# Kernel optimization log

Hardware: AMD Instinct MI355X
Metric: run time of the kernel (lower is better)

Reference implementation:

```python
import jax, jax.numpy as jnp
import numpy as np

SOS, EOS, PAD = 1, 2, 0


def setup_inputs() -> dict:
    key = jax.random.key(0)
    ks = jax.random.split(key, 8)
    n, d_z, d_h, d_emb, V = 8192, 128, 512, 128, 64
    s = lambda k, shape, scale: jax.random.normal(k, shape, jnp.float32) * scale
    return {
        "Z": jax.random.normal(ks[0], (n, d_z), jnp.float32),
        "emb": s(ks[1], (V, d_emb), 0.1),
        "z2h_w": s(ks[2], (d_h, d_z), 0.05),
        "z2h_b": jnp.zeros((d_h,), jnp.float32),
        "w_ih0": s(ks[3], (3 * d_h, d_emb), 0.05),
        "w_ih_rest": s(ks[4], (2, 3 * d_h, d_h), 0.05),
        "w_hh": s(ks[5], (3, 3 * d_h, d_h), 0.05),
        "b_ih": jnp.zeros((3, 3 * d_h), jnp.float32),
        "b_hh": jnp.zeros((3, 3 * d_h), jnp.float32),
        "h2v_w": s(ks[6], (V, d_h), 0.05),
        "h2v_b": jnp.zeros((V,), jnp.float32),
        "max_len": 80,
    }


def _gru_cell(x, h, w_ih, w_hh, b_ih, b_hh):
    # torch GRU gate order: r, z, n
    gi = x @ w_ih.T + b_ih
    gh = h @ w_hh.T + b_hh
    i_r, i_z, i_n = jnp.split(gi, 3, axis=-1)
    h_r, h_z, h_n = jnp.split(gh, 3, axis=-1)
    r = jax.nn.sigmoid(i_r + h_r)
    z = jax.nn.sigmoid(i_z + h_z)
    g = jnp.tanh(i_n + r * h_n)
    return (1.0 - z) * g + z * h


def _decode(Z, emb, z2h_w, z2h_b, w_ih0, w_ih_rest, w_hh, b_ih, b_hh, h2v_w, h2v_b, max_len):
    n = Z.shape[0]
    L = w_hh.shape[0]
    h0 = Z @ z2h_w.T + z2h_b                      # [n, d_h], repeated over layers
    H = jnp.broadcast_to(h0[None], (L,) + h0.shape)
    x0 = jnp.full((n,), SOS, jnp.int32)
    eos0 = jnp.zeros((n,), bool)
    w_ih = [w_ih0] + [w_ih_rest[i] for i in range(w_ih_rest.shape[0])]

    def step(carry, t):
        H, x_prev, eos = carry
        inp = emb[x_prev]                          # [n, d_emb]
        Hs = []
        for l in range(L):                         # small fixed layer loop
            h_new = _gru_cell(inp, H[l], w_ih[l], w_hh[l], b_ih[l], b_hh[l])
            Hs.append(h_new)
            inp = h_new
        probs = jax.nn.softmax(inp @ h2v_w.T + h2v_b, axis=-1)  # [n, V]
        x_t = jnp.argmax(probs, axis=-1).astype(jnp.int32)      # ModeSampler
        tok = jnp.where(eos, PAD, x_t)             # masked write into X_gen
        new_eos = (~eos) & (x_t == EOS)
        return (jnp.stack(Hs), x_t, eos | new_eos), (tok, new_eos, probs)

    ts = jnp.arange(1, max_len, dtype=jnp.int32)
    _, (toks, new_eos, probs) = jax.lax.scan(step, (H, x0, eos0), ts)
    X_gen = jnp.concatenate([jnp.full((n, 1), SOS, jnp.int32), toks.T], axis=1)  # [n, max_len]
    any_eos = new_eos.any(axis=0)
    first_t = ts[jnp.argmax(new_eos, axis=0)]
    seq_lens = jnp.where(any_eos, first_t + 1, max_len).astype(jnp.int32)
    return X_gen, seq_lens, probs


def reference(Z, emb, z2h_w, z2h_b, w_ih0, w_ih_rest, w_hh, b_ih, b_hh, h2v_w, h2v_b, max_len):
    X_gen, seq_lens, _ = _decode(Z, emb, z2h_w, z2h_b, w_ih0, w_ih_rest,
                                 w_hh, b_ih, b_hh, h2v_w, h2v_b, max_len)
    # torch returns a ragged list X_gen[i, :seq_lens[i]]; we return the padded
    # tensor plus lengths (jit-compatible equivalent).
    return X_gen, seq_lens
```

## Files before the change

### kernel.cpp

```cpp
#include <hip/hip_runtime.h>
#include <math.h>

#define NSEQ 8192
#define DH 512
#define DZ 128
#define DE 128
#define VOCAB 64
#define TMAX 80
#define SOS 1
#define EOS_TOK 2

#define TMR 64
#define TNCOL 32

typedef _Float16 half_t;
typedef half_t h8 __attribute__((ext_vector_type(8)));
typedef float f4 __attribute__((ext_vector_type(4)));

__device__ __forceinline__ float sigf(float x) { return 1.0f / (1.0f + expf(-x)); }

__device__ __forceinline__ void split2(float v, half_t& hi, half_t& lo) {
    float hf = (float)(half_t)v;
    if (fabsf(v) < 6.2e-5f) hf = 0.0f;
    hi = (half_t)hf;
    lo = (half_t)((v - hf) * 2048.0f);
}

__device__ __forceinline__ float rec2(half_t h, half_t l) {
    return (float)h + (float)l * (1.0f / 2048.0f);
}

__device__ __forceinline__ void gl_lds16(const void* g, void* l) {
    __builtin_amdgcn_global_load_lds((const __attribute__((address_space(1))) void*)g,
                                     (__attribute__((address_space(3))) void*)l, 16, 0, 0);
}

__device__ __forceinline__ void swizzle_rc(int bid, int& r, int& c) {
    const int x = bid & 7;
    const int q = bid >> 3;
    r = (q & 15) * 8 + x;
    c = q >> 4;
}

__global__ __launch_bounds__(256) void init_kernel(int* __restrict__ x_prev,
                                                   int* __restrict__ eos,
                                                   int* __restrict__ out,
                                                   int* __restrict__ list,
                                                   int* __restrict__ count) {
    int i = blockIdx.x * 256 + threadIdx.x;
    x_prev[i] = SOS;
    eos[i] = 0;
    list[i] = i;
    out[i * TMAX] = SOS;
    out[NSEQ * TMAX + i] = TMAX;
    if (i == 0) count[0] = NSEQ;
}

__global__ __launch_bounds__(1024) void compact_kernel(const int* __restrict__ eos,
                                                       int* __restrict__ list,
                                                       int* __restrict__ count) {
    __shared__ int part[1024];
    __shared__ int slist[NSEQ];
    const int tid = threadIdx.x;
    const int base = tid * 8;
    int f[8], s = 0;
#pragma unroll
    for (int i = 0; i < 8; ++i) { f[i] = eos[base + i] ? 0 : 1; s += f[i]; }
    part[tid] = s;
    __syncthreads();
    for (int off = 1; off < 1024; off <<= 1) {
        int v = (tid >= off) ? part[tid - off] : 0;
        __syncthreads();
        part[tid] += v;
        __syncthreads();
    }
    const int total = part[1023];
    int p = part[tid] - s;
#pragma unroll
    for (int i = 0; i < 8; ++i) if (f[i]) slist[p++] = base + i;
    __syncthreads();
    if (tid == 0) {
        count[0] = total;
        if (total > 0) {
            const int last = slist[total - 1];
            const int padn = (total + 63) & ~63;
            for (int k = total; k < padn; ++k) slist[k] = last;
        }
    }
    __syncthreads();
    const int padn = (total + 63) & ~63;
    for (int k = tid; k < padn; k += 1024) list[k] = slist[k];
}

__global__ __launch_bounds__(256) void h0_kernel(const float* __restrict__ Z,
                                                 const float* __restrict__ w,
                                                 const float* __restrict__ b,
                                                 half_t* __restrict__ B0h, half_t* __restrict__ B0l,
                                                 half_t* __restrict__ B1h, half_t* __restrict__ B1l,
                                                 half_t* __restrict__ B2h, half_t* __restrict__ B2l) {
    __shared__ float zrow[DZ];
    const int i = blockIdx.x;
    const int tid = threadIdx.x;
    if (tid < DZ) zrow[tid] = Z[(size_t)i * DZ + tid];
    __syncthreads();
    for (int j = tid; j < DH; j += 256) {
        double s = (double)b[j];
        const float* wr = w + (size_t)j * DZ;
#pragma unroll 8
        for (int k = 0; k < DZ; ++k) s += (double)zrow[k] * (double)wr[k];
        float sf = (float)s;
        half_t hi, lo;
        split2(sf, hi, lo);
        size_t o = (size_t)i * DH + j;
        B0h[o] = hi; B0l[o] = lo;
        B1h[o] = hi; B1l[o] = lo;
        B2h[o] = hi; B2l[o] = lo;
    }
}

__global__ __launch_bounds__(256) void gi0_kernel(const float* __restrict__ emb,
                                                  const float* __restrict__ w_ih0,
                                                  const float* __restrict__ b_ih0,
                                                  double* __restrict__ tab) {
    __shared__ float e[DE];
    const int x = blockIdx.x;
    const int tid = threadIdx.x;
    if (tid < DE) e[tid] = emb[(size_t)x * DE + tid];
    __syncthreads();
    for (int j = tid; j < 3 * DH; j += 256) {
        double s = (double)b_ih0[j];
        const float* wr = w_ih0 + (size_t)j * DE;
#pragma unroll 8
        for (int k = 0; k < DE; ++k) s += (double)e[k] * (double)wr[k];
        tab[(size_t)x * 3 * DH + j] = s;
    }
}

__global__ __launch_bounds__(256) void wsplit_kernel(const float* __restrict__ w,
                                                     half_t* __restrict__ hi,
                                                     half_t* __restrict__ lo, int n) {
    int i = blockIdx.x * 256 + threadIdx.x;
    if (i < n) {
        half_t h, l;
        split2(w[i], h, l);
        hi[i] = h; lo[i] = l;
    }
}


__global__ __launch_bounds__(256, 3) void layer0_mfma(
    const half_t* __restrict__ Hch, const half_t* __restrict__ Hcl,
    half_t* __restrict__ Hnh, half_t* __restrict__ Hnl,
    const half_t* __restrict__ Wh, const half_t* __restrict__ Wl,
    const float* __restrict__ b_hh0,
    const double* __restrict__ tab,
    const int* __restrict__ x_prev,
    const int* __restrict__ list, const int* __restrict__ count) {
    int rt, ct;
    swizzle_rc(blockIdx.x, rt, ct);
    const int row0 = rt * TMR;
    const int cnt = count[0];
    if (row0 >= cnt) return;
    const int col0 = ct * TNCOL;

    __shared__ char sm[40960];
    const int tid = threadIdx.x;
    const int lane = tid & 63, w = tid >> 6;
    const int lr = lane & 15, lq = lane >> 4;
    const int wr0 = (w >> 1) * 32, wc0 = (w & 1) * 16;

    int aoff[2], boff[3];
#pragma unroll
    for (int i = 0; i < 2; ++i) {
        int u = i * 256 + tid, r = u >> 3, s = u & 7;
        aoff[i] = list[row0 + r] * 1024 + ((s ^ (r & 7)) << 4);
    }
#pragma unroll
    for (int j = 0; j < 3; ++j) {
        int u = j * 256 + tid, br = u >> 3, s = u & 7;
        int wr = (br >> 5) * DH + col0 + (br & 31);
        boff[j] = wr * 1024 + ((s ^ (br & 7)) << 4);
    }

    int fa[2][2], fb[3][2];
#pragma unroll
    for (int rf = 0; rf < 2; ++rf)
#pragma unroll
        for (int ks = 0; ks < 2; ++ks) {
            int row = wr0 + rf * 16 + lr;
            int sb = ks * 4 + lq;
            fa[rf][ks] = row * 128 + ((sb ^ (row & 7)) << 4);
        }
#pragma unroll
    for (int g = 0; g < 3; ++g)
#pragma unroll
        for (int ks = 0; ks < 2; ++ks) {
            int br = g * 32 + wc0 + lr;
            int sb = ks * 4 + lq;
            fb[g][ks] = br * 128 + ((sb ^ (br & 7)) << 4);
        }

    f4 hh[2][3] = {}, cc[2][3] = {};
    const char* Ah = (const char*)Hch;
    const char* Al = (const char*)Hcl;
    const char* Bh = (const char*)Wh;
    const char* Bl = (const char*)Wl;

    for (int kc = 0; kc < 8; ++kc) {
        const int kb = kc * 128;
#pragma unroll
        for (int i = 0; i < 2; ++i) {
            gl_lds16(Ah + aoff[i] + kb, sm + (i * 256 + tid) * 16);
            gl_lds16(Al + aoff[i] + kb, sm + 8192 + (i * 256 + tid) * 16);
        }
#pragma unroll
        for (int j = 0; j < 3; ++j) {
            gl_lds16(Bh + boff[j] + kb, sm + 16384 + (j * 256 + tid) * 16);
            gl_lds16(Bl + boff[j] + kb, sm + 28672 + (j * 256 + tid) * 16);
        }
        __syncthreads();
#pragma unroll
        for (int ks = 0; ks < 2; ++ks) {
            h8 a0h = *(const h8*)(sm + fa[0][ks]);
            h8 a0l = *(const h8*)(sm + 8192 + fa[0][ks]);
            h8 a1h = *(const h8*)(sm + fa[1][ks]);
            h8 a1l = *(const h8*)(sm + 8192 + fa[1][ks]);
#pragma unroll
            for (int g = 0; g < 3; ++g) {
                h8 bh = *(const h8*)(sm + 16384 + fb[g][ks]);
                h8 bl = *(const h8*)(sm + 28672 + fb[g][ks]);
                hh[0][g] = __builtin_amdgcn_mfma_f32_16x16x32_f16(a0h, bh, hh[0][g], 0, 0, 0);
                cc[0][g] = __builtin_amdgcn_mfma_f32_16x16x32_f16(a0h, bl, cc[0][g], 0, 0, 0);
                cc[0][g] = __builtin_amdgcn_mfma_f32_16x16x32_f16(a0l, bh, cc[0][g], 0, 0, 0);
                hh[1][g] = __builtin_amdgcn_mfma_f32_16x16x32_f16(a1h, bh, hh[1][g], 0, 0, 0);
                cc[1][g] = __builtin_amdgcn_mfma_f32_16x16x32_f16(a1h, bl, cc[1][g], 0, 0, 0);
                cc[1][g] = __builtin_amdgcn_mfma_f32_16x16x32_f16(a1l, bh, cc[1][g], 0, 0, 0);
            }
        }
        __syncthreads();
    }

    const float inv = 1.0f / 2048.0f;
#pragma unroll
    for (int rf = 0; rf < 2; ++rf) {
        f4 pR = hh[rf][0] + cc[rf][0] * inv;
        f4 pZ = hh[rf][1] + cc[rf][1] * inv;
        f4 pN = hh[rf][2] + cc[rf][2] * inv;
        const int gj = col0 + wc0 + lr;
#pragma unroll
        for (int reg = 0; reg < 4; ++reg) {
            const int rl = wr0 + rf * 16 + lq * 4 + reg;
            const int gi = list[row0 + rl];
            const double* tr = tab + (size_t)x_prev[gi] * (3 * DH);
            float xr = (float)(tr[gj] + (double)pR[reg] + (double)b_hh0[gj]);
            float xz = (float)(tr[DH + gj] + (double)pZ[reg] + (double)b_hh0[DH + gj]);
            float hn_pre = pN[reg] + b_hh0[2 * DH + gj];
            float r = sigf(xr), z = sigf(xz);
            float g = tanhf((float)(tr[2 * DH + gj] + (double)r * (double)hn_pre));
            size_t o = (size_t)gi * DH + gj;
            float ho = rec2(Hch[o], Hcl[o]);
            float h = (1.0f - z) * g + z * ho;
            half_t oh, ol;
            split2(h, oh, ol);
            Hnh[o] = oh; Hnl[o] = ol;
        }
    }
}

__global__ __launch_bounds__(256, 3) void layer12_mfma(
    const half_t* __restrict__ Xh, const half_t* __restrict__ Xl,
    const half_t* __restrict__ Hch, const half_t* __restrict__ Hcl,
    half_t* __restrict__ Hnh, half_t* __restrict__ Hnl,
    const half_t* __restrict__ Wih_h, const half_t* __restrict__ Wih_l,
    const half_t* __restrict__ Whh_h, const half_t* __restrict__ Whh_l,
    const float* __restrict__ b_ih, const float* __restrict__ b_hh,
    const int* __restrict__ list, const int* __restrict__ count) {
    int rt, ct;
    swizzle_rc(blockIdx.x, rt, ct);
    const int row0 = rt * TMR;
    const int cnt = count[0];
    if (row0 >= cnt) return;
    const int col0 = ct * TNCOL;

    __shared__ char sm[40960];
    const int tid = threadIdx.x;
    const int lane = tid & 63, w = tid >> 6;
    const int lr = lane & 15, lq = lane >> 4;
    const int wr0 = (w >> 1) * 32, wc0 = (w & 1) * 16;

    int aoff[2], boff[3];
#pragma unroll
    for (int i = 0; i < 2; ++i) {
        int u = i * 256 + tid, r = u >> 3, s = u & 7;
        aoff[i] = list[row0 + r] * 1024 + ((s ^ (r & 7)) << 4);
    }
#pragma unroll
    for (int j = 0; j < 3; ++j) {
        int u = j * 256 + tid, br = u >> 3, s = u & 7;
        int wr = (br >> 5) * DH + col0 + (br & 31);
        boff[j] = wr * 1024 + ((s ^ (br & 7)) << 4);
    }

    int fa[2][2], fb[3][2];
#pragma unroll
    for (int rf = 0; rf < 2; ++rf)
#pragma unroll
        for (int ks = 0; ks < 2; ++ks) {
            int row = wr0 + rf * 16 + lr;
            int sb = ks * 4 + lq;
            fa[rf][ks] = row * 128 + ((sb ^ (row & 7)) << 4);
        }
#pragma unroll
    for (int g = 0; g < 3; ++g)
#pragma unroll
        for (int ks = 0; ks < 2; ++ks) {
            int br = g * 32 + wc0 + lr;
            int sb = ks * 4 + lq;
            fb[g][ks] = br * 128 + ((sb ^ (br & 7)) << 4);
        }

    f4 hh[2][3] = {}, cc[2][3] = {}, niS[2] = {};

    for (int kc = 0; kc < 16; ++kc) {
        const int kb = (kc & 7) * 128;
        const char* As_h = (kc < 8) ? (const char*)Xh : (const char*)Hch;
        const char* As_l = (kc < 8) ? (const char*)Xl : (const char*)Hcl;
        const char* Ws_h = (kc < 8) ? (const char*)Wih_h : (const char*)Whh_h;
        const char* Ws_l = (kc < 8) ? (const char*)Wih_l : (const char*)Whh_l;
#pragma unroll
        for (int i = 0; i < 2; ++i) {
            gl_lds16(As_h + aoff[i] + kb, sm + (i * 256 + tid) * 16);
            gl_lds16(As_l + aoff[i] + kb, sm + 8192 + (i * 256 + tid) * 16);
        }
#pragma unroll
        for (int j = 0; j < 3; ++j) {
            gl_lds16(Ws_h + boff[j] + kb, sm + 16384 + (j * 256 + tid) * 16);
            gl_lds16(Ws_l + boff[j] + kb, sm + 28672 + (j * 256 + tid) * 16);
        }
        __syncthreads();
#pragma unroll
        for (int ks = 0; ks < 2; ++ks) {
            h8 a0h = *(const h8*)(sm + fa[0][ks]);
            h8 a0l = *(const h8*)(sm + 8192 + fa[0][ks]);
            h8 a1h = *(const h8*)(sm + fa[1][ks]);
            h8 a1l = *(const h8*)(sm + 8192 + fa[1][ks]);
#pragma unroll
            for (int g = 0; g < 3; ++g) {
                h8 bh = *(const h8*)(sm + 16384 + fb[g][ks]);
                h8 bl = *(const h8*)(sm + 28672 + fb[g][ks]);
                hh[0][g] = __builtin_amdgcn_mfma_f32_16x16x32_f16(a0h, bh, hh[0][g], 0, 0, 0);
                cc[0][g] = __builtin_amdgcn_mfma_f32_16x16x32_f16(a0h, bl, cc[0][g], 0, 0, 0);
                cc[0][g] = __builtin_amdgcn_mfma_f32_16x16x32_f16(a0l, bh, cc[0][g], 0, 0, 0);
                hh[1][g] = __builtin_amdgcn_mfma_f32_16x16x32_f16(a1h, bh, hh[1][g], 0, 0, 0);
                cc[1][g] = __builtin_amdgcn_mfma_f32_16x16x32_f16(a1h, bl, cc[1][g], 0, 0, 0);
                cc[1][g] = __builtin_amdgcn_mfma_f32_16x16x32_f16(a1l, bh, cc[1][g], 0, 0, 0);
            }
        }
        __syncthreads();
        if (kc == 7) {
#pragma unroll
            for (int rf = 0; rf < 2; ++rf) {
                niS[rf] = hh[rf][2] + cc[rf][2] * (1.0f / 2048.0f);
                f4 zz = {0.0f, 0.0f, 0.0f, 0.0f};
                hh[rf][2] = zz;
                cc[rf][2] = zz;
            }
        }
    }

    const float inv = 1.0f / 2048.0f;
#pragma unroll
    for (int rf = 0; rf < 2; ++rf) {
        f4 pR = hh[rf][0] + cc[rf][0] * inv;
        f4 pZ = hh[rf][1] + cc[rf][1] * inv;
        f4 pNH = hh[rf][2] + cc[rf][2] * inv;
        f4 pNI = niS[rf];
        const int gj = col0 + wc0 + lr;
#pragma unroll
        for (int reg = 0; reg < 4; ++reg) {
            const int rl = wr0 + rf * 16 + lq * 4 + reg;
            const int gi = list[row0 + rl];
            float xr = pR[reg] + b_ih[gj] + b_hh[gj];
            float xz = pZ[reg] + b_ih[DH + gj] + b_hh[DH + gj];
            float xi = pNI[reg] + b_ih[2 * DH + gj];
            float hn_pre = pNH[reg] + b_hh[2 * DH + gj];
            float r = sigf(xr), z = sigf(xz);
            float g = tanhf(xi + r * hn_pre);
            size_t o = (size_t)gi * DH + gj;
            float ho = rec2(Hch[o], Hcl[o]);
            float h = (1.0f - z) * g + z * ho;
            half_t oh, ol;
            split2(h, oh, ol);
            Hnh[o] = oh; Hnl[o] = ol;
        }
    }
}

__global__ __launch_bounds__(256) void logits_kernel(const half_t* __restrict__ H2h,
                                                     const half_t* __restrict__ H2l,
                                                     const float* __restrict__ h2v_w,
                                                     const float* __restrict__ h2v_b,
                                                     int* __restrict__ x_prev,
                                                     int* __restrict__ eos,
                                                     int* __restrict__ out,
                                                     const int* __restrict__ list,
                                                     const int* __restrict__ count,
                                                     int t) {
    const int rowbase = blockIdx.x * 16;
    const int cnt = count[0];
    if (rowbase >= cnt) return;

    __shared__ float Ws[VOCAB][65];
    __shared__ float Hs[16][65];
    const int tid = threadIdx.x;
    double acc[4] = {0.0, 0.0, 0.0, 0.0};

    for (int k0 = 0; k0 < DH; k0 += 64) {
        __syncthreads();
#pragma unroll
        for (int it = 0; it < 16; ++it) {
            int idx = tid + 256 * it;
            int v = idx >> 6, k = idx & 63;
            Ws[v][k] = h2v_w[(size_t)v * DH + k0 + k];
        }
#pragma unroll
        for (int it = 0; it < 4; ++it) {
            int idx = tid + 256 * it;
            int r = idx >> 6, k = idx & 63;
            size_t o = (size_t)list[rowbase + r] * DH + k0 + k;
            Hs[r][k] = rec2(H2h[o], H2l[o]);
        }
        __syncthreads();
        const int r = tid >> 4;
        const int vb = (tid & 15) * 4;
#pragma unroll 16
        for (int k = 0; k < 64; ++k) {
            double h = (double)Hs[r][k];
            acc[0] += h * (double)Ws[vb + 0][k];
            acc[1] += h * (double)Ws[vb + 1][k];
            acc[2] += h * (double)Ws[vb + 2][k];
            acc[3] += h * (double)Ws[vb + 3][k];
        }
    }

    const int r = tid >> 4;
    const int vb = (tid & 15) * 4;
    float lf[4];
#pragma unroll
    for (int vv = 0; vv < 4; ++vv) lf[vv] = (float)(acc[vv] + (double)h2v_b[vb + vv]);

    float m = fmaxf(fmaxf(lf[0], lf[1]), fmaxf(lf[2], lf[3]));
#pragma unroll
    for (int off = 1; off < 16; off <<= 1) m = fmaxf(m, __shfl_xor(m, off));
    float e[4];
    float ssum = 0.f;
#pragma unroll
    for (int vv = 0; vv < 4; ++vv) { e[vv] = expf(lf[vv] - m); ssum += e[vv]; }
#pragma unroll
    for (int off = 1; off < 16; off <<= 1) ssum += __shfl_xor(ssum, off);

    float best = e[0] / ssum;
    int bi = vb;
#pragma unroll
    for (int vv = 1; vv < 4; ++vv) {
        float pv = e[vv] / ssum;
        if (pv > best) { best = pv; bi = vb + vv; }
    }
#pragma unroll
    for (int off = 1; off < 16; off <<= 1) {
        float ov = __shfl_xor(best, off);
        int oi = __shfl_xor(bi, off);
        if (ov > best || (ov == best && oi < bi)) { best = ov; bi = oi; }
    }
    if ((tid & 15) == 0) {
        const int gi = list[rowbase + r];
        const int ee = eos[gi];
        const int xt = bi;
        out[(size_t)gi * TMAX + t] = ee ? 0 : xt;
        if (!ee && xt == EOS_TOK) {
            out[NSEQ * TMAX + gi] = t + 1;
            eos[gi] = 1;
        }
        x_prev[gi] = xt;
    }
}

extern "C" void kernel_launch(void* const* d_in, const int* in_sizes, int n_in,
                              void* d_out, int out_size, void* d_ws, size_t ws_size,
                              hipStream_t stream) {
    const float* Z        = (const float*)d_in[0];
    const float* emb      = (const float*)d_in[1];
    const float* z2h_w    = (const float*)d_in[2];
    const float* z2h_b    = (const float*)d_in[3];
    const float* w_ih0    = (const float*)d_in[4];
    const float* w_ih_rest= (const float*)d_in[5];
    const float* w_hh     = (const float*)d_in[6];
    const float* b_ih     = (const float*)d_in[7];
    const float* b_hh     = (const float*)d_in[8];
    const float* h2v_w    = (const float*)d_in[9];
    const float* h2v_b    = (const float*)d_in[10];

    int* out = (int*)d_out;
    char* p = (char*)d_ws;
    const size_t HS = (size_t)NSEQ * DH * sizeof(half_t);
    half_t* Bh[4]; half_t* Bl[4];
    for (int i = 0; i < 4; ++i) { Bh[i] = (half_t*)p; p += HS; }
    for (int i = 0; i < 4; ++i) { Bl[i] = (half_t*)p; p += HS; }
    double* tab = (double*)p; p += (size_t)VOCAB * 3 * DH * sizeof(double);
    const size_t WH = (size_t)3 * DH * DH;
    half_t* wih_h = (half_t*)p; p += 2 * WH * sizeof(half_t);
    half_t* wih_l = (half_t*)p; p += 2 * WH * sizeof(half_t);
    half_t* whh_h = (half_t*)p; p += 3 * WH * sizeof(half_t);
    half_t* whh_l = (half_t*)p; p += 3 * WH * sizeof(half_t);
    int* x_prev = (int*)p; p += NSEQ * sizeof(int);
    int* eos    = (int*)p; p += NSEQ * sizeof(int);
    int* alist  = (int*)p; p += NSEQ * sizeof(int);
    int* acount = (int*)p; p += 256;

    hipMemsetAsync(out, 0, (size_t)NSEQ * TMAX * sizeof(int), stream);
    init_kernel<<<NSEQ / 256, 256, 0, stream>>>(x_prev, eos, out, alist, acount);
    h0_kernel<<<NSEQ, 256, 0, stream>>>(Z, z2h_w, z2h_b,
                                        Bh[0], Bl[0], Bh[1], Bl[1], Bh[2], Bl[2]);
    gi0_kernel<<<VOCAB, 256, 0, stream>>>(emb, w_ih0, b_ih, tab);
    wsplit_kernel<<<(int)((2 * WH + 255) / 256), 256, 0, stream>>>(w_ih_rest, wih_h, wih_l, (int)(2 * WH));
    wsplit_kernel<<<(int)((3 * WH + 255) / 256), 256, 0, stream>>>(w_hh, whh_h, whh_l, (int)(3 * WH));

    int c0 = 0, c1 = 1, c2 = 2, sp = 3;
    const int lgrid = (NSEQ / TMR) * (DH / TNCOL);
    for (int t = 1; t < TMAX; ++t) {
        layer0_mfma<<<lgrid, 256, 0, stream>>>(Bh[c0], Bl[c0], Bh[sp], Bl[sp],
            whh_h, whh_l, b_hh, tab, x_prev, alist, acount);
        layer12_mfma<<<lgrid, 256, 0, stream>>>(Bh[sp], Bl[sp], Bh[c1], Bl[c1], Bh[c0], Bl[c0],
            wih_h, wih_l, whh_h + WH, whh_l + WH, b_ih + 3 * DH, b_hh + 3 * DH, alist, acount);
        layer12_mfma<<<lgrid, 256, 0, stream>>>(Bh[c0], Bl[c0], Bh[c2], Bl[c2], Bh[c1], Bl[c1],
            wih_h + WH, wih_l + WH, whh_h + 2 * WH, whh_l + 2 * WH,
            b_ih + 6 * DH, b_hh + 6 * DH, alist, acount);
        logits_kernel<<<NSEQ / 16, 256, 0, stream>>>(Bh[c1], Bl[c1], h2v_w, h2v_b,
                                                     x_prev, eos, out, alist, acount, t);
        if (t < TMAX - 1)
            compact_kernel<<<1, 1024, 0, stream>>>(eos, alist, acount);
        int n0 = sp, n1 = c0, n2 = c1, nsp = c2;
        c0 = n0; c1 = n1; c2 = n2; sp = nsp;
    }
}
```

Before: 14.98 ms.

## Double-buffer weight tiles, load activations to registers, fuse list compaction into logits

The GRU MFMA kernels now double-buffer the weight tiles in LDS. They load the gathered hidden-state A fragments straight into registers instead of staging them through LDS, and use manual waitcnt/barrier scheduling so the next k-chunk's loads overlap the current chunk's MFMAs. The separate single-block compaction kernel is removed. Active-row lists are now built in the logits kernel through per-block atomicAdd into ping-pong list and count buffers, which removes one launch and a serial scan per step. In exchange, list order becomes nondeterministic, rows beyond the count are clamped, and more registers are used, which may lower occupancy.

```diff
diff --git a/kernel.cpp b/kernel.cpp
--- a/kernel.cpp
+++ b/kernel.cpp
@@ -45,51 +45,15 @@
 __global__ __launch_bounds__(256) void init_kernel(int* __restrict__ x_prev,
                                                    int* __restrict__ eos,
                                                    int* __restrict__ out,
-                                                   int* __restrict__ list,
-                                                   int* __restrict__ count) {
+                                                   int* __restrict__ list0,
+                                                   int* __restrict__ counts) {
     int i = blockIdx.x * 256 + threadIdx.x;
     x_prev[i] = SOS;
     eos[i] = 0;
-    list[i] = i;
+    list0[i] = i;
     out[i * TMAX] = SOS;
     out[NSEQ * TMAX + i] = TMAX;
-    if (i == 0) count[0] = NSEQ;
-}
-
-__global__ __launch_bounds__(1024) void compact_kernel(const int* __restrict__ eos,
-                                                       int* __restrict__ list,
-                                                       int* __restrict__ count) {
-    __shared__ int part[1024];
-    __shared__ int slist[NSEQ];
-    const int tid = threadIdx.x;
-    const int base = tid * 8;
-    int f[8], s = 0;
-#pragma unroll
-    for (int i = 0; i < 8; ++i) { f[i] = eos[base + i] ? 0 : 1; s += f[i]; }
-    part[tid] = s;
-    __syncthreads();
-    for (int off = 1; off < 1024; off <<= 1) {
-        int v = (tid >= off) ? part[tid - off] : 0;
-        __syncthreads();
-        part[tid] += v;
-        __syncthreads();
-    }
-    const int total = part[1023];
-    int p = part[tid] - s;
-#pragma unroll
-    for (int i = 0; i < 8; ++i) if (f[i]) slist[p++] = base + i;
-    __syncthreads();
-    if (tid == 0) {
-        count[0] = total;
-        if (total > 0) {
-            const int last = slist[total - 1];
-            const int padn = (total + 63) & ~63;
-            for (int k = total; k < padn; ++k) slist[k] = last;
-        }
-    }
-    __syncthreads();
-    const int padn = (total + 63) & ~63;
-    for (int k = tid; k < padn; k += 1024) list[k] = slist[k];
+    if (i < TMAX) counts[i] = (i == 0) ? NSEQ : 0;
 }
 
 __global__ __launch_bounds__(256) void h0_kernel(const float* __restrict__ Z,
@@ -163,105 +127,116 @@
     if (row0 >= cnt) return;
     const int col0 = ct * TNCOL;
 
-    __shared__ char sm[40960];
+    __shared__ __align__(16) char sm[49152];
     const int tid = threadIdx.x;
     const int lane = tid & 63, w = tid >> 6;
     const int lr = lane & 15, lq = lane >> 4;
     const int wr0 = (w >> 1) * 32, wc0 = (w & 1) * 16;
 
-    int aoff[2], boff[3];
-#pragma unroll
-    for (int i = 0; i < 2; ++i) {
-        int u = i * 256 + tid, r = u >> 3, s = u & 7;
-        aoff[i] = list[row0 + r] * 1024 + ((s ^ (r & 7)) << 4);
-    }
+    unsigned bsrc[3]; int bldsu[3];
 #pragma unroll
     for (int j = 0; j < 3; ++j) {
         int u = j * 256 + tid, br = u >> 3, s = u & 7;
-        int wr = (br >> 5) * DH + col0 + (br & 31);
-        boff[j] = wr * 1024 + ((s ^ (br & 7)) << 4);
-    }
-
-    int fa[2][2], fb[3][2];
-#pragma unroll
-    for (int rf = 0; rf < 2; ++rf)
-#pragma unroll
-        for (int ks = 0; ks < 2; ++ks) {
-            int row = wr0 + rf * 16 + lr;
-            int sb = ks * 4 + lq;
-            fa[rf][ks] = row * 128 + ((sb ^ (row & 7)) << 4);
-        }
+        bsrc[j] = (unsigned)(((br >> 5) * DH + col0 + (br & 31)) * 1024 + ((s ^ (br & 7)) << 4));
+        bldsu[j] = u * 16;
+    }
+    int fb[3][2];
 #pragma unroll
     for (int g = 0; g < 3; ++g)
 #pragma unroll
         for (int ks = 0; ks < 2; ++ks) {
             int br = g * 32 + wc0 + lr;
-            int sb = ks * 4 + lq;
-            fb[g][ks] = br * 128 + ((sb ^ (br & 7)) << 4);
-        }
+            fb[g][ks] = br * 128 + (((ks * 4 + lq) ^ (br & 7)) << 4);
+        }
+    unsigned abase[2];
+#pragma unroll
+    for (int rf = 0; rf < 2; ++rf) {
+        int ri = row0 + wr0 + rf * 16 + lr;
+        if (ri > cnt - 1) ri = cnt - 1;
+        abase[rf] = (unsigned)list[ri] * 1024u + (unsigned)(lq * 16);
+    }
 
     f4 hh[2][3] = {}, cc[2][3] = {};
-    const char* Ah = (const char*)Hch;
-    const char* Al = (const char*)Hcl;
-    const char* Bh = (const char*)Wh;
-    const char* Bl = (const char*)Wl;
-
-    for (int kc = 0; kc < 8; ++kc) {
-        const int kb = kc * 128;
-#pragma unroll
-        for (int i = 0; i < 2; ++i) {
-            gl_lds16(Ah + aoff[i] + kb, sm + (i * 256 + tid) * 16);
-            gl_lds16(Al + aoff[i] + kb, sm + 8192 + (i * 256 + tid) * 16);
-        }
+
+    auto stageB = [&](int bb, int kc) {
+        const unsigned ko = (unsigned)kc * 128u;
 #pragma unroll
         for (int j = 0; j < 3; ++j) {
-            gl_lds16(Bh + boff[j] + kb, sm + 16384 + (j * 256 + tid) * 16);
-            gl_lds16(Bl + boff[j] + kb, sm + 28672 + (j * 256 + tid) * 16);
-        }
-        __syncthreads();
-#pragma unroll
-        for (int ks = 0; ks < 2; ++ks) {
-            h8 a0h = *(const h8*)(sm + fa[0][ks]);
-            h8 a0l = *(const h8*)(sm + 8192 + fa[0][ks]);
-            h8 a1h = *(const h8*)(sm + fa[1][ks]);
-            h8 a1l = *(const h8*)(sm + 8192 + fa[1][ks]);
+            gl_lds16((const char*)Wh + (size_t)(bsrc[j] + ko), sm + bb + bldsu[j]);
+            gl_lds16((const char*)Wl + (size_t)(bsrc[j] + ko), sm + bb + 12288 + bldsu[j]);
+        }
+    };
+    auto loadA = [&](h8* d, int kc) {
+        const unsigned ko = (unsigned)kc * 128u;
+#pragma unroll
+        for (int rf = 0; rf < 2; ++rf)
+#pragma unroll
+            for (int ks = 0; ks < 2; ++ks) {
+                const size_t off = (size_t)(abase[rf] + ko + (unsigned)(ks * 64));
+                d[rf * 4 + ks * 2 + 0] = *(const h8*)((const char*)Hch + off);
+                d[rf * 4 + ks * 2 + 1] = *(const h8*)((const char*)Hcl + off);
+            }
+    };
+    auto compute = [&](int bb, const h8* A) {
+#pragma unroll
+        for (int ks = 0; ks < 2; ++ks)
 #pragma unroll
             for (int g = 0; g < 3; ++g) {
-                h8 bh = *(const h8*)(sm + 16384 + fb[g][ks]);
-                h8 bl = *(const h8*)(sm + 28672 + fb[g][ks]);
-                hh[0][g] = __builtin_amdgcn_mfma_f32_16x16x32_f16(a0h, bh, hh[0][g], 0, 0, 0);
-                cc[0][g] = __builtin_amdgcn_mfma_f32_16x16x32_f16(a0h, bl, cc[0][g], 0, 0, 0);
-                cc[0][g] = __builtin_amdgcn_mfma_f32_16x16x32_f16(a0l, bh, cc[0][g], 0, 0, 0);
-                hh[1][g] = __builtin_amdgcn_mfma_f32_16x16x32_f16(a1h, bh, hh[1][g], 0, 0, 0);
-                cc[1][g] = __builtin_amdgcn_mfma_f32_16x16x32_f16(a1h, bl, cc[1][g], 0, 0, 0);
-                cc[1][g] = __builtin_amdgcn_mfma_f32_16x16x32_f16(a1l, bh, cc[1][g], 0, 0, 0);
+                h8 bh = *(const h8*)(sm + bb + fb[g][ks]);
+                h8 bl = *(const h8*)(sm + bb + 12288 + fb[g][ks]);
+#pragma unroll
+                for (int rf = 0; rf < 2; ++rf) {
+                    hh[rf][g] = __builtin_amdgcn_mfma_f32_16x16x32_f16(A[rf * 4 + ks * 2], bh, hh[rf][g], 0, 0, 0);
+                    cc[rf][g] = __builtin_amdgcn_mfma_f32_16x16x32_f16(A[rf * 4 + ks * 2], bl, cc[rf][g], 0, 0, 0);
+                    cc[rf][g] = __builtin_amdgcn_mfma_f32_16x16x32_f16(A[rf * 4 + ks * 2 + 1], bh, cc[rf][g], 0, 0, 0);
+                }
             }
-        }
-        __syncthreads();
-    }
-
+    };
+
+    h8 A0[8], A1[8];
+    stageB(0, 0); loadA(A0, 0);
+    for (int kc = 0; kc < 8; kc += 2) {
+        stageB(24576, kc + 1); loadA(A1, kc + 1);
+        asm volatile("s_waitcnt vmcnt(14)" ::: "memory");
+        asm volatile("s_barrier" ::: "memory");
+        compute(0, A0);
+        asm volatile("s_waitcnt lgkmcnt(0)" ::: "memory");
+        asm volatile("s_barrier" ::: "memory");
+        if (kc + 2 < 8) {
+            stageB(0, kc + 2); loadA(A0, kc + 2);
+            asm volatile("s_waitcnt vmcnt(14)" ::: "memory");
+        } else {
+            asm volatile("s_waitcnt vmcnt(0)" ::: "memory");
+        }
+        asm volatile("s_barrier" ::: "memory");
+        compute(24576, A1);
+        asm volatile("s_waitcnt lgkmcnt(0)" ::: "memory");
+        asm volatile("s_barrier" ::: "memory");
+    }
+
+    const int colg = col0 + wc0 + lr;
     const float inv = 1.0f / 2048.0f;
 #pragma unroll
     for (int rf = 0; rf < 2; ++rf) {
         f4 pR = hh[rf][0] + cc[rf][0] * inv;
         f4 pZ = hh[rf][1] + cc[rf][1] * inv;
         f4 pN = hh[rf][2] + cc[rf][2] * inv;
-        const int gj = col0 + wc0 + lr;
 #pragma unroll
         for (int reg = 0; reg < 4; ++reg) {
-            const int rl = wr0 + rf * 16 + lq * 4 + reg;
-            const int gi = list[row0 + rl];
+            int ri = row0 + wr0 + rf * 16 + lq * 4 + reg;
+            if (ri > cnt - 1) ri = cnt - 1;
+            const int gi = list[ri];
             const double* tr = tab + (size_t)x_prev[gi] * (3 * DH);
-            float xr = (float)(tr[gj] + (double)pR[reg] + (double)b_hh0[gj]);
-            float xz = (float)(tr[DH + gj] + (double)pZ[reg] + (double)b_hh0[DH + gj]);
-            float hn_pre = pN[reg] + b_hh0[2 * DH + gj];
-            float r = sigf(xr), z = sigf(xz);
-            float g = tanhf((float)(tr[2 * DH + gj] + (double)r * (double)hn_pre));
-            size_t o = (size_t)gi * DH + gj;
+            float xr = (float)(tr[colg] + (double)pR[reg] + (double)b_hh0[colg]);
+            float xz = (float)(tr[DH + colg] + (double)pZ[reg] + (double)b_hh0[DH + colg]);
+            float hn_pre = pN[reg] + b_hh0[2 * DH + colg];
+            float rg = sigf(xr), zg = sigf(xz);
+            float gg = tanhf((float)(tr[2 * DH + colg] + (double)rg * (double)hn_pre));
+            size_t o = (size_t)gi * DH + colg;
             float ho = rec2(Hch[o], Hcl[o]);
-            float h = (1.0f - z) * g + z * ho;
+            float hv = (1.0f - zg) * gg + zg * ho;
             half_t oh, ol;
-            split2(h, oh, ol);
+            split2(hv, oh, ol);
             Hnh[o] = oh; Hnl[o] = ol;
         }
     }
@@ -282,115 +257,128 @@
     if (row0 >= cnt) return;
     const int col0 = ct * TNCOL;
 
-    __shared__ char sm[40960];
+    __shared__ __align__(16) char sm[49152];
     const int tid = threadIdx.x;
     const int lane = tid & 63, w = tid >> 6;
     const int lr = lane & 15, lq = lane >> 4;
     const int wr0 = (w >> 1) * 32, wc0 = (w & 1) * 16;
 
-    int aoff[2], boff[3];
-#pragma unroll
-    for (int i = 0; i < 2; ++i) {
-        int u = i * 256 + tid, r = u >> 3, s = u & 7;
-        aoff[i] = list[row0 + r] * 1024 + ((s ^ (r & 7)) << 4);
-    }
+    unsigned bsrc[3]; int bldsu[3];
 #pragma unroll
     for (int j = 0; j < 3; ++j) {
         int u = j * 256 + tid, br = u >> 3, s = u & 7;
-        int wr = (br >> 5) * DH + col0 + (br & 31);
-        boff[j] = wr * 1024 + ((s ^ (br & 7)) << 4);
-    }
-
-    int fa[2][2], fb[3][2];
-#pragma unroll
-    for (int rf = 0; rf < 2; ++rf)
-#pragma unroll
-        for (int ks = 0; ks < 2; ++ks) {
-            int row = wr0 + rf * 16 + lr;
-            int sb = ks * 4 + lq;
-            fa[rf][ks] = row * 128 + ((sb ^ (row & 7)) << 4);
-        }
+        bsrc[j] = (unsigned)(((br >> 5) * DH + col0 + (br & 31)) * 1024 + ((s ^ (br & 7)) << 4));
+        bldsu[j] = u * 16;
+    }
+    int fb[3][2];
 #pragma unroll
     for (int g = 0; g < 3; ++g)
 #pragma unroll
         for (int ks = 0; ks < 2; ++ks) {
             int br = g * 32 + wc0 + lr;
-            int sb = ks * 4 + lq;
-            fb[g][ks] = br * 128 + ((sb ^ (br & 7)) << 4);
-        }
+            fb[g][ks] = br * 128 + (((ks * 4 + lq) ^ (br & 7)) << 4);
+        }
+    unsigned abase[2];
+#pragma unroll
+    for (int rf = 0; rf < 2; ++rf) {
+        int ri = row0 + wr0 + rf * 16 + lr;
+        if (ri > cnt - 1) ri = cnt - 1;
+        abase[rf] = (unsigned)list[ri] * 1024u + (unsigned)(lq * 16);
+    }
 
     f4 hh[2][3] = {}, cc[2][3] = {}, niS[2] = {};
 
-    for (int kc = 0; kc < 16; ++kc) {
-        const int kb = (kc & 7) * 128;
-        const char* As_h = (kc < 8) ? (const char*)Xh : (const char*)Hch;
-        const char* As_l = (kc < 8) ? (const char*)Xl : (const char*)Hcl;
-        const char* Ws_h = (kc < 8) ? (const char*)Wih_h : (const char*)Whh_h;
-        const char* Ws_l = (kc < 8) ? (const char*)Wih_l : (const char*)Whh_l;
-#pragma unroll
-        for (int i = 0; i < 2; ++i) {
-            gl_lds16(As_h + aoff[i] + kb, sm + (i * 256 + tid) * 16);
-            gl_lds16(As_l + aoff[i] + kb, sm + 8192 + (i * 256 + tid) * 16);
-        }
+    auto stageB = [&](int bb, int kc) {
+        const half_t* Bh_ = (kc < 8) ? Wih_h : Whh_h;
+        const half_t* Bl_ = (kc < 8) ? Wih_l : Whh_l;
+        const unsigned ko = (unsigned)(kc & 7) * 128u;
 #pragma unroll
         for (int j = 0; j < 3; ++j) {
-            gl_lds16(Ws_h + boff[j] + kb, sm + 16384 + (j * 256 + tid) * 16);
-            gl_lds16(Ws_l + boff[j] + kb, sm + 28672 + (j * 256 + tid) * 16);
-        }
-        __syncthreads();
-#pragma unroll
-        for (int ks = 0; ks < 2; ++ks) {
-            h8 a0h = *(const h8*)(sm + fa[0][ks]);
-            h8 a0l = *(const h8*)(sm + 8192 + fa[0][ks]);
-            h8 a1h = *(const h8*)(sm + fa[1][ks]);
-            h8 a1l = *(const h8*)(sm + 8192 + fa[1][ks]);
+            gl_lds16((const char*)Bh_ + (size_t)(bsrc[j] + ko), sm + bb + bldsu[j]);
+            gl_lds16((const char*)Bl_ + (size_t)(bsrc[j] + ko), sm + bb + 12288 + bldsu[j]);
+        }
+    };
+    auto loadA = [&](h8* d, int kc) {
+        const char* Ah_ = (kc < 8) ? (const char*)Xh : (const char*)Hch;
+        const char* Al_ = (kc < 8) ? (const char*)Xl : (const char*)Hcl;
+        const unsigned ko = (unsigned)(kc & 7) * 128u;
+#pragma unroll
+        for (int rf = 0; rf < 2; ++rf)
+#pragma unroll
+            for (int ks = 0; ks < 2; ++ks) {
+                const size_t off = (size_t)(abase[rf] + ko + (unsigned)(ks * 64));
+                d[rf * 4 + ks * 2 + 0] = *(const h8*)(Ah_ + off);
+                d[rf * 4 + ks * 2 + 1] = *(const h8*)(Al_ + off);
+            }
+    };
+    auto compute = [&](int bb, const h8* A) {
+#pragma unroll
+        for (int ks = 0; ks < 2; ++ks)
 #pragma unroll
             for (int g = 0; g < 3; ++g) {
-                h8 bh = *(const h8*)(sm + 16384 + fb[g][ks]);
-                h8 bl = *(const h8*)(sm + 28672 + fb[g][ks]);
-                hh[0][g] = __builtin_amdgcn_mfma_f32_16x16x32_f16(a0h, bh, hh[0][g], 0, 0, 0);
-                cc[0][g] = __builtin_amdgcn_mfma_f32_16x16x32_f16(a0h, bl, cc[0][g], 0, 0, 0);
-                cc[0][g] = __builtin_amdgcn_mfma_f32_16x16x32_f16(a0l, bh, cc[0][g], 0, 0, 0);
-                hh[1][g] = __builtin_amdgcn_mfma_f32_16x16x32_f16(a1h, bh, hh[1][g], 0, 0, 0);
-                cc[1][g] = __builtin_amdgcn_mfma_f32_16x16x32_f16(a1h, bl, cc[1][g], 0, 0, 0);
-                cc[1][g] = __builtin_amdgcn_mfma_f32_16x16x32_f16(a1l, bh, cc[1][g], 0, 0, 0);
+                h8 bh = *(const h8*)(sm + bb + fb[g][ks]);
+                h8 bl = *(const h8*)(sm + bb + 12288 + fb[g][ks]);
+#pragma unroll
+                for (int rf = 0; rf < 2; ++rf) {
+                    hh[rf][g] = __builtin_amdgcn_mfma_f32_16x16x32_f16(A[rf * 4 + ks * 2], bh, hh[rf][g], 0, 0, 0);
+                    cc[rf][g] = __builtin_amdgcn_mfma_f32_16x16x32_f16(A[rf * 4 + ks * 2], bl, cc[rf][g], 0, 0, 0);
+                    cc[rf][g] = __builtin_amdgcn_mfma_f32_16x16x32_f16(A[rf * 4 + ks * 2 + 1], bh, cc[rf][g], 0, 0, 0);
+                }
             }
-        }
-        __syncthreads();
-        if (kc == 7) {
+    };
+
+    h8 A0[8], A1[8];
+    stageB(0, 0); loadA(A0, 0);
+    for (int kc = 0; kc < 16; kc += 2) {
+        stageB(24576, kc + 1); loadA(A1, kc + 1);
+        asm volatile("s_waitcnt vmcnt(14)" ::: "memory");
+        asm volatile("s_barrier" ::: "memory");
+        compute(0, A0);
+        asm volatile("s_waitcnt lgkmcnt(0)" ::: "memory");
+        asm volatile("s_barrier" ::: "memory");
+        if (kc + 2 < 16) {
+            stageB(0, kc + 2); loadA(A0, kc + 2);
+            asm volatile("s_waitcnt vmcnt(14)" ::: "memory");
+        } else {
+            asm volatile("s_waitcnt vmcnt(0)" ::: "memory");
+        }
+        asm volatile("s_barrier" ::: "memory");
+        compute(24576, A1);
+        if (kc == 6) {
 #pragma unroll
             for (int rf = 0; rf < 2; ++rf) {
                 niS[rf] = hh[rf][2] + cc[rf][2] * (1.0f / 2048.0f);
                 f4 zz = {0.0f, 0.0f, 0.0f, 0.0f};
-                hh[rf][2] = zz;
-                cc[rf][2] = zz;
+                hh[rf][2] = zz; cc[rf][2] = zz;
             }
         }
-    }
-
+        asm volatile("s_waitcnt lgkmcnt(0)" ::: "memory");
+        asm volatile("s_barrier" ::: "memory");
+    }
+
+    const int colg = col0 + wc0 + lr;
     const float inv = 1.0f / 2048.0f;
 #pragma unroll
     for (int rf = 0; rf < 2; ++rf) {
         f4 pR = hh[rf][0] + cc[rf][0] * inv;
         f4 pZ = hh[rf][1] + cc[rf][1] * inv;
         f4 pNH = hh[rf][2] + cc[rf][2] * inv;
-        f4 pNI = niS[rf];
-        const int gj = col0 + wc0 + lr;
 #pragma unroll
         for (int reg = 0; reg < 4; ++reg) {
-            const int rl = wr0 + rf * 16 + lq * 4 + reg;
-            const int gi = list[row0 + rl];
-            float xr = pR[reg] + b_ih[gj] + b_hh[gj];
-            float xz = pZ[reg] + b_ih[DH + gj] + b_hh[DH + gj];
-            float xi = pNI[reg] + b_ih[2 * DH + gj];
-            float hn_pre = pNH[reg] + b_hh[2 * DH + gj];
-            float r = sigf(xr), z = sigf(xz);
-            float g = tanhf(xi + r * hn_pre);
-            size_t o = (size_t)gi * DH + gj;
+            int ri = row0 + wr0 + rf * 16 + lq * 4 + reg;
+            if (ri > cnt - 1) ri = cnt - 1;
+            const int gi = list[ri];
+            float xr = pR[reg] + b_ih[colg] + b_hh[colg];
+            float xz = pZ[reg] + b_ih[DH + colg] + b_hh[DH + colg];
+            float xi = niS[rf][reg] + b_ih[2 * DH + colg];
+            float hn_pre = pNH[reg] + b_hh[2 * DH + colg];
+            float rg = sigf(xr), zg = sigf(xz);
+            float gg = tanhf(xi + rg * hn_pre);
+            size_t o = (size_t)gi * DH + colg;
             float ho = rec2(Hch[o], Hcl[o]);
-            float h = (1.0f - z) * g + z * ho;
+            float hv = (1.0f - zg) * gg + zg * ho;
             half_t oh, ol;
-            split2(h, oh, ol);
+            split2(hv, oh, ol);
             Hnh[o] = oh; Hnl[o] = ol;
         }
     }
@@ -405,6 +393,8 @@
                                                      int* __restrict__ out,
                                                      const int* __restrict__ list,
                                                      const int* __restrict__ count,
+                                                     int* __restrict__ list_next,
+                                                     int* __restrict__ count_next,
                                                      int t) {
     const int rowbase = blockIdx.x * 16;
     const int cnt = count[0];
@@ -412,6 +402,7 @@
 
     __shared__ float Ws[VOCAB][65];
     __shared__ float Hs[16][65];
+    __shared__ int sact[16];
     const int tid = threadIdx.x;
     double acc[4] = {0.0, 0.0, 0.0, 0.0};
 
@@ -427,7 +418,8 @@
         for (int it = 0; it < 4; ++it) {
             int idx = tid + 256 * it;
             int r = idx >> 6, k = idx & 63;
-            size_t o = (size_t)list[rowbase + r] * DH + k0 + k;
+            int pos = rowbase + r; if (pos > cnt - 1) pos = cnt - 1;
+            size_t o = (size_t)list[pos] * DH + k0 + k;
             Hs[r][k] = rec2(H2h[o], H2l[o]);
         }
         __syncthreads();
@@ -473,15 +465,30 @@
         if (ov > best || (ov == best && oi < bi)) { best = ov; bi = oi; }
     }
     if ((tid & 15) == 0) {
-        const int gi = list[rowbase + r];
+        const int pos = rowbase + r;
+        const bool valid = pos < cnt;
+        const int gi = list[valid ? pos : (cnt - 1)];
         const int ee = eos[gi];
         const int xt = bi;
-        out[(size_t)gi * TMAX + t] = ee ? 0 : xt;
-        if (!ee && xt == EOS_TOK) {
-            out[NSEQ * TMAX + gi] = t + 1;
-            eos[gi] = 1;
-        }
-        x_prev[gi] = xt;
+        if (valid) {
+            out[(size_t)gi * TMAX + t] = ee ? 0 : xt;
+            if (!ee && xt == EOS_TOK) {
+                out[NSEQ * TMAX + gi] = t + 1;
+                eos[gi] = 1;
+            }
+            x_prev[gi] = xt;
+        }
+        sact[r] = (valid && !ee && xt != EOS_TOK) ? gi : -1;
+    }
+    __syncthreads();
+    if (tid == 0) {
+        int loc[16], k = 0;
+#pragma unroll
+        for (int i = 0; i < 16; ++i) { int v = sact[i]; if (v >= 0) loc[k++] = v; }
+        if (k > 0) {
+            int b = atomicAdd(count_next, k);
+            for (int i = 0; i < k; ++i) list_next[b + i] = loc[i];
+        }
     }
 }
 
@@ -514,11 +521,13 @@
     half_t* whh_l = (half_t*)p; p += 3 * WH * sizeof(half_t);
     int* x_prev = (int*)p; p += NSEQ * sizeof(int);
     int* eos    = (int*)p; p += NSEQ * sizeof(int);
-    int* alist  = (int*)p; p += NSEQ * sizeof(int);
-    int* acount = (int*)p; p += 256;
+    int* lists[2];
+    lists[0] = (int*)p; p += NSEQ * sizeof(int);
+    lists[1] = (int*)p; p += NSEQ * sizeof(int);
+    int* counts = (int*)p; p += 128 * sizeof(int);
 
     hipMemsetAsync(out, 0, (size_t)NSEQ * TMAX * sizeof(int), stream);
-    init_kernel<<<NSEQ / 256, 256, 0, stream>>>(x_prev, eos, out, alist, acount);
+    init_kernel<<<NSEQ / 256, 256, 0, stream>>>(x_prev, eos, out, lists[0], counts);
     h0_kernel<<<NSEQ, 256, 0, stream>>>(Z, z2h_w, z2h_b,
                                         Bh[0], Bl[0], Bh[1], Bl[1], Bh[2], Bl[2]);
     gi0_kernel<<<VOCAB, 256, 0, stream>>>(emb, w_ih0, b_ih, tab);
@@ -528,17 +537,18 @@
     int c0 = 0, c1 = 1, c2 = 2, sp = 3;
     const int lgrid = (NSEQ / TMR) * (DH / TNCOL);
     for (int t = 1; t < TMAX; ++t) {
+        const int* lcur = lists[(t - 1) & 1];
+        const int* ccur = counts + (t - 1);
         layer0_mfma<<<lgrid, 256, 0, stream>>>(Bh[c0], Bl[c0], Bh[sp], Bl[sp],
-            whh_h, whh_l, b_hh, tab, x_prev, alist, acount);
+            whh_h, whh_l, b_hh, tab, x_prev, lcur, ccur);
         layer12_mfma<<<lgrid, 256, 0, stream>>>(Bh[sp], Bl[sp], Bh[c1], Bl[c1], Bh[c0], Bl[c0],
-            wih_h, wih_l, whh_h + WH, whh_l + WH, b_ih + 3 * DH, b_hh + 3 * DH, alist, acount);
+            wih_h, wih_l, whh_h + WH, whh_l + WH, b_ih + 3 * DH, b_hh + 3 * DH, lcur, ccur);
         layer12_mfma<<<lgrid, 256, 0, stream>>>(Bh[c0], Bl[c0], Bh[c2], Bl[c2], Bh[c1], Bl[c1],
             wih_h + WH, wih_l + WH, whh_h + 2 * WH, whh_l + 2 * WH,
-            b_ih + 6 * DH, b_hh + 6 * DH, alist, acount);
+            b_ih + 6 * DH, b_hh + 6 * DH, lcur, ccur);
         logits_kernel<<<NSEQ / 16, 256, 0, stream>>>(Bh[c1], Bl[c1], h2v_w, h2v_b,
-                                                     x_prev, eos, out, alist, acount, t);
-        if (t < TMAX - 1)
-            compact_kernel<<<1, 1024, 0, stream>>>(eos, alist, acount);
+                                                     x_prev, eos, out, lcur, ccur,
+                                                     lists[t & 1], counts + t, t);
         int n0 = sp, n1 = c0, n2 = c1, nsp = c2;
         c0 = n0; c1 = n1; c2 = n2; sp = nsp;
     }
```

New measurement: 25.46 ms. 70.0% more time.

## Fuse active-list compaction into logits kernel via atomic append

Applied to the files above, without the earlier changes.

Removes the separate single-block compact_kernel launched every step. The logits kernel now appends still-active sequence indices to a double-buffered next list through a per-block atomicAdd, with a separate count slot per timestep. The GEMM kernels clamp out-of-range rows to the last valid entry instead of relying on padded lists. This saves one serialized 1024-thread launch per step, but list order becomes nondeterministic, which can reduce gather locality.

```diff
diff --git a/kernel.cpp b/kernel.cpp
--- a/kernel.cpp
+++ b/kernel.cpp
@@ -45,51 +45,15 @@
 __global__ __launch_bounds__(256) void init_kernel(int* __restrict__ x_prev,
                                                    int* __restrict__ eos,
                                                    int* __restrict__ out,
-                                                   int* __restrict__ list,
-                                                   int* __restrict__ count) {
+                                                   int* __restrict__ list0,
+                                                   int* __restrict__ counts) {
     int i = blockIdx.x * 256 + threadIdx.x;
     x_prev[i] = SOS;
     eos[i] = 0;
-    list[i] = i;
+    list0[i] = i;
     out[i * TMAX] = SOS;
     out[NSEQ * TMAX + i] = TMAX;
-    if (i == 0) count[0] = NSEQ;
-}
-
-__global__ __launch_bounds__(1024) void compact_kernel(const int* __restrict__ eos,
-                                                       int* __restrict__ list,
-                                                       int* __restrict__ count) {
-    __shared__ int part[1024];
-    __shared__ int slist[NSEQ];
-    const int tid = threadIdx.x;
-    const int base = tid * 8;
-    int f[8], s = 0;
-#pragma unroll
-    for (int i = 0; i < 8; ++i) { f[i] = eos[base + i] ? 0 : 1; s += f[i]; }
-    part[tid] = s;
-    __syncthreads();
-    for (int off = 1; off < 1024; off <<= 1) {
-        int v = (tid >= off) ? part[tid - off] : 0;
-        __syncthreads();
-        part[tid] += v;
-        __syncthreads();
-    }
-    const int total = part[1023];
-    int p = part[tid] - s;
-#pragma unroll
-    for (int i = 0; i < 8; ++i) if (f[i]) slist[p++] = base + i;
-    __syncthreads();
-    if (tid == 0) {
-        count[0] = total;
-        if (total > 0) {
-            const int last = slist[total - 1];
-            const int padn = (total + 63) & ~63;
-            for (int k = total; k < padn; ++k) slist[k] = last;
-        }
-    }
-    __syncthreads();
-    const int padn = (total + 63) & ~63;
-    for (int k = tid; k < padn; k += 1024) list[k] = slist[k];
+    if (i < TMAX) counts[i] = (i == 0) ? NSEQ : 0;
 }
 
 __global__ __launch_bounds__(256) void h0_kernel(const float* __restrict__ Z,
@@ -173,7 +137,8 @@
 #pragma unroll
     for (int i = 0; i < 2; ++i) {
         int u = i * 256 + tid, r = u >> 3, s = u & 7;
-        aoff[i] = list[row0 + r] * 1024 + ((s ^ (r & 7)) << 4);
+        int rr = row0 + r; if (rr > cnt - 1) rr = cnt - 1;
+        aoff[i] = list[rr] * 1024 + ((s ^ (r & 7)) << 4);
     }
 #pragma unroll
     for (int j = 0; j < 3; ++j) {
@@ -249,8 +214,9 @@
         const int gj = col0 + wc0 + lr;
 #pragma unroll
         for (int reg = 0; reg < 4; ++reg) {
-            const int rl = wr0 + rf * 16 + lq * 4 + reg;
-            const int gi = list[row0 + rl];
+            int pos = row0 + wr0 + rf * 16 + lq * 4 + reg;
+            if (pos > cnt - 1) pos = cnt - 1;
+            const int gi = list[pos];
             const double* tr = tab + (size_t)x_prev[gi] * (3 * DH);
             float xr = (float)(tr[gj] + (double)pR[reg] + (double)b_hh0[gj]);
             float xz = (float)(tr[DH + gj] + (double)pZ[reg] + (double)b_hh0[DH + gj]);
@@ -292,7 +258,8 @@
 #pragma unroll
     for (int i = 0; i < 2; ++i) {
         int u = i * 256 + tid, r = u >> 3, s = u & 7;
-        aoff[i] = list[row0 + r] * 1024 + ((s ^ (r & 7)) << 4);
+        int rr = row0 + r; if (rr > cnt - 1) rr = cnt - 1;
+        aoff[i] = list[rr] * 1024 + ((s ^ (r & 7)) << 4);
     }
 #pragma unroll
     for (int j = 0; j < 3; ++j) {
@@ -378,8 +345,9 @@
         const int gj = col0 + wc0 + lr;
 #pragma unroll
         for (int reg = 0; reg < 4; ++reg) {
-            const int rl = wr0 + rf * 16 + lq * 4 + reg;
-            const int gi = list[row0 + rl];
+            int pos = row0 + wr0 + rf * 16 + lq * 4 + reg;
+            if (pos > cnt - 1) pos = cnt - 1;
+            const int gi = list[pos];
             float xr = pR[reg] + b_ih[gj] + b_hh[gj];
             float xz = pZ[reg] + b_ih[DH + gj] + b_hh[DH + gj];
             float xi = pNI[reg] + b_ih[2 * DH + gj];
@@ -405,6 +373,8 @@
                                                      int* __restrict__ out,
                                                      const int* __restrict__ list,
                                                      const int* __restrict__ count,
+                                                     int* __restrict__ list_next,
+                                                     int* __restrict__ count_next,
                                                      int t) {
     const int rowbase = blockIdx.x * 16;
     const int cnt = count[0];
@@ -412,6 +382,7 @@
 
     __shared__ float Ws[VOCAB][65];
     __shared__ float Hs[16][65];
+    __shared__ int sact[16];
     const int tid = threadIdx.x;
     double acc[4] = {0.0, 0.0, 0.0, 0.0};
 
@@ -427,7 +398,8 @@
         for (int it = 0; it < 4; ++it) {
             int idx = tid + 256 * it;
             int r = idx >> 6, k = idx & 63;
-            size_t o = (size_t)list[rowbase + r] * DH + k0 + k;
+            int pos = rowbase + r; if (pos > cnt - 1) pos = cnt - 1;
+            size_t o = (size_t)list[pos] * DH + k0 + k;
             Hs[r][k] = rec2(H2h[o], H2l[o]);
         }
         __syncthreads();
@@ -473,15 +445,30 @@
         if (ov > best || (ov == best && oi < bi)) { best = ov; bi = oi; }
     }
     if ((tid & 15) == 0) {
-        const int gi = list[rowbase + r];
+        const int pos = rowbase + r;
+        const bool valid = pos < cnt;
+        const int gi = list[valid ? pos : (cnt - 1)];
         const int ee = eos[gi];
         const int xt = bi;
-        out[(size_t)gi * TMAX + t] = ee ? 0 : xt;
-        if (!ee && xt == EOS_TOK) {
-            out[NSEQ * TMAX + gi] = t + 1;
-            eos[gi] = 1;
-        }
-        x_prev[gi] = xt;
+        if (valid) {
+            out[(size_t)gi * TMAX + t] = ee ? 0 : xt;
+            if (!ee && xt == EOS_TOK) {
+                out[NSEQ * TMAX + gi] = t + 1;
+                eos[gi] = 1;
+            }
+            x_prev[gi] = xt;
+        }
+        sact[r] = (valid && !ee && xt != EOS_TOK) ? gi : -1;
+    }
+    __syncthreads();
+    if (tid == 0) {
+        int loc[16], k = 0;
+#pragma unroll
+        for (int i = 0; i < 16; ++i) { int v = sact[i]; if (v >= 0) loc[k++] = v; }
+        if (k > 0) {
+            int b = atomicAdd(count_next, k);
+            for (int i = 0; i < k; ++i) list_next[b + i] = loc[i];
+        }
     }
 }
 
@@ -514,11 +501,13 @@
     half_t* whh_l = (half_t*)p; p += 3 * WH * sizeof(half_t);
     int* x_prev = (int*)p; p += NSEQ * sizeof(int);
     int* eos    = (int*)p; p += NSEQ * sizeof(int);
-    int* alist  = (int*)p; p += NSEQ * sizeof(int);
-    int* acount = (int*)p; p += 256;
+    int* lists[2];
+    lists[0] = (int*)p; p += NSEQ * sizeof(int);
+    lists[1] = (int*)p; p += NSEQ * sizeof(int);
+    int* counts = (int*)p; p += 128 * sizeof(int);
 
     hipMemsetAsync(out, 0, (size_t)NSEQ * TMAX * sizeof(int), stream);
-    init_kernel<<<NSEQ / 256, 256, 0, stream>>>(x_prev, eos, out, alist, acount);
+    init_kernel<<<NSEQ / 256, 256, 0, stream>>>(x_prev, eos, out, lists[0], counts);
     h0_kernel<<<NSEQ, 256, 0, stream>>>(Z, z2h_w, z2h_b,
                                         Bh[0], Bl[0], Bh[1], Bl[1], Bh[2], Bl[2]);
     gi0_kernel<<<VOCAB, 256, 0, stream>>>(emb, w_ih0, b_ih, tab);
@@ -528,17 +517,18 @@
     int c0 = 0, c1 = 1, c2 = 2, sp = 3;
     const int lgrid = (NSEQ / TMR) * (DH / TNCOL);
     for (int t = 1; t < TMAX; ++t) {
+        const int* lcur = lists[(t - 1) & 1];
+        const int* ccur = counts + (t - 1);
         layer0_mfma<<<lgrid, 256, 0, stream>>>(Bh[c0], Bl[c0], Bh[sp], Bl[sp],
-            whh_h, whh_l, b_hh, tab, x_prev, alist, acount);
+            whh_h, whh_l, b_hh, tab, x_prev, lcur, ccur);
         layer12_mfma<<<lgrid, 256, 0, stream>>>(Bh[sp], Bl[sp], Bh[c1], Bl[c1], Bh[c0], Bl[c0],
-            wih_h, wih_l, whh_h + WH, whh_l + WH, b_ih + 3 * DH, b_hh + 3 * DH, alist, acount);
+            wih_h, wih_l, whh_h + WH, whh_l + WH, b_ih + 3 * DH, b_hh + 3 * DH, lcur, ccur);
         layer12_mfma<<<lgrid, 256, 0, stream>>>(Bh[c0], Bl[c0], Bh[c2], Bl[c2], Bh[c1], Bl[c1],
             wih_h + WH, wih_l + WH, whh_h + 2 * WH, whh_l + 2 * WH,
-            b_ih + 6 * DH, b_hh + 6 * DH, alist, acount);
+            b_ih + 6 * DH, b_hh + 6 * DH, lcur, ccur);
         logits_kernel<<<NSEQ / 16, 256, 0, stream>>>(Bh[c1], Bl[c1], h2v_w, h2v_b,
-                                                     x_prev, eos, out, alist, acount, t);
-        if (t < TMAX - 1)
-            compact_kernel<<<1, 1024, 0, stream>>>(eos, alist, acount);
+                                                     x_prev, eos, out, lcur, ccur,
+                                                     lists[t & 1], counts + t, t);
         int n0 = sp, n1 = c0, n2 = c1, nsp = c2;
         c0 = n0; c1 = n1; c2 = n2; sp = nsp;
     }
```

After: 14.82 ms, median of 2. No clear change (-1.1%).
